# Kernel tuning notes

Measured on AMD Instinct MI355X. Metric: run time of the kernel, lower is better.

The kernel has to match this reference:

```python
import jax, jax.numpy as jnp
import numpy as np

N = 100000   # nodes
E = 1_600_000  # edges (avg degree 16)
D = 64       # input_dim = hidden_dim = output_dim
EPS = 1e-5   # BatchNorm eps


def setup_inputs() -> dict:
    key = jax.random.key(0)
    ks = jax.random.split(key, 8)
    x = jax.random.normal(ks[0], (N, D), jnp.float32)
    edge_index = jax.random.randint(ks[1], (2, E), 0, N, jnp.int32)

    def lin_w(k, din, dout):
        s = 1.0 / np.sqrt(din)
        return jax.random.uniform(k, (din, dout), jnp.float32, -s, s)

    return {
        "x": x, "edge_index": edge_index,
        "W1": lin_w(ks[2], D, D), "b1": jnp.zeros((D,), jnp.float32),
        "g1": jnp.ones((D,), jnp.float32), "be1": jnp.zeros((D,), jnp.float32),
        "W2": lin_w(ks[3], D, D), "b2": jnp.zeros((D,), jnp.float32),
        "g2": jnp.ones((D,), jnp.float32), "be2": jnp.zeros((D,), jnp.float32),
        "W3": lin_w(ks[4], D, D), "b3": jnp.zeros((D,), jnp.float32),
        "g3": jnp.ones((D,), jnp.float32), "be3": jnp.zeros((D,), jnp.float32),
    }


def gcn_conv(x, src, dst, W, b):
    # GCNConv: out = D^{-1/2}(A+I)D^{-1/2} (x @ W) + b
    n = x.shape[0]
    loops = jnp.arange(n, dtype=src.dtype)
    s = jnp.concatenate([src, loops])  # add self-loops
    d = jnp.concatenate([dst, loops])
    deg = jax.ops.segment_sum(jnp.ones_like(s, jnp.float32), d, num_segments=n)
    dinv = jax.lax.rsqrt(jnp.maximum(deg, 1.0))  # deg >= 1 (self-loops)
    norm = dinv[s] * dinv[d]                     # [E+N]
    xw = x @ W                                   # [N, D]
    msgs = xw[s] * norm[:, None]                 # [E+N, D] gather
    return jax.ops.segment_sum(msgs, d, num_segments=n) + b  # scatter-add


def batch_norm(z, g, be):
    # training-mode BatchNorm1d: batch statistics, biased variance
    mu = jnp.mean(z, axis=0)
    var = jnp.mean(jnp.square(z - mu), axis=0)
    return (z - mu) * jax.lax.rsqrt(var + EPS) * g + be


def reference(x, edge_index, W1, b1, g1, be1, W2, b2, g2, be2, W3, b3, g3, be3):
    src, dst = edge_index[0], edge_index[1]
    z = jax.nn.relu(batch_norm(gcn_conv(x, src, dst, W1, b1), g1, be1))
    z = jax.nn.relu(batch_norm(gcn_conv(z, src, dst, W2, b2), g2, be2))
    z = batch_norm(gcn_conv(z, src, dst, W3, b3), g3, be3)
    # dropout (p=0.1) is identity in eval mode; normalize=False default
    return z
```

## Files before the change

### kernel.cpp

```cpp
#include <hip/hip_runtime.h>

typedef unsigned short ushort_t;
typedef unsigned int uint_t;
typedef float f32x4 __attribute__((ext_vector_type(4)));
typedef short bf16x8 __attribute__((ext_vector_type(8)));

#define NB_AGG 2560
#define BSHIFT 7
#define BROWS 128
#define BCAP 4096
#define NCHUNK 256
#define ZP 72

__device__ __forceinline__ float bf2f_lo(uint_t u) {
    union { uint_t i; float f; } v; v.i = u << 16; return v.f;
}
__device__ __forceinline__ float bf2f_hi(uint_t u) {
    union { uint_t i; float f; } v; v.i = u & 0xffff0000u; return v.f;
}
__device__ __forceinline__ ushort_t f2bf(float f) {
    union { float f; uint_t i; } v; v.f = f;
    uint_t u = v.i;
    uint_t r = (u + 0x7fffu + ((u >> 16) & 1u)) >> 16;
    return (ushort_t)r;
}

__global__ __launch_bounds__(256) void hist2_k(const int* __restrict__ dst,
                                               int* __restrict__ H, int E, int nb) {
    __shared__ int h[1024];
    int b = blockIdx.x, t = threadIdx.x;
    for (int i = t; i < nb; i += 256) h[i] = 0;
    __syncthreads();
    int per = (E + NCHUNK - 1) / NCHUNK;
    int lo = b * per, hi = min(E, lo + per);
    for (int e = lo + t; e < hi; e += 256)
        atomicAdd(&h[dst[e] >> BSHIFT], 1);
    __syncthreads();
    for (int i = t; i < nb; i += 256) H[(size_t)i * NCHUNK + b] = h[i];
}

__global__ __launch_bounds__(256) void scanA_k(const int* __restrict__ v,
                                               int* __restrict__ segsum, int total) {
    int base = blockIdx.x * 1024 + threadIdx.x;
    int s = 0;
#pragma unroll
    for (int i = 0; i < 4; ++i) {
        int idx = base + i * 256;
        if (idx < total) s += v[idx];
    }
    __shared__ int sh[256];
    sh[threadIdx.x] = s;
    __syncthreads();
    for (int off = 128; off > 0; off >>= 1) {
        if (threadIdx.x < off) sh[threadIdx.x] += sh[threadIdx.x + off];
        __syncthreads();
    }
    if (threadIdx.x == 0) segsum[blockIdx.x] = sh[0];
}

__global__ void scanB_k(int* segsum, int nseg) {
    __shared__ int sh[256];
    int t = threadIdx.x;
    int own = (t < nseg) ? segsum[t] : 0;
    sh[t] = own;
    __syncthreads();
    for (int off = 1; off < 256; off <<= 1) {
        int v = (t >= off) ? sh[t - off] : 0;
        __syncthreads();
        sh[t] += v;
        __syncthreads();
    }
    if (t < nseg) segsum[t] = sh[t] - own;
}

__global__ __launch_bounds__(256) void scanC2_k(int* __restrict__ H,
                                                const int* __restrict__ segsum,
                                                int total) {
    int t = threadIdx.x;
    int base = blockIdx.x * 1024 + t * 4;
    int c0 = 0, c1 = 0, c2 = 0, c3 = 0;
    if (base + 0 < total) c0 = H[base + 0];
    if (base + 1 < total) c1 = H[base + 1];
    if (base + 2 < total) c2 = H[base + 2];
    if (base + 3 < total) c3 = H[base + 3];
    int tsum = c0 + c1 + c2 + c3;
    __shared__ int sh[256];
    sh[t] = tsum;
    __syncthreads();
    for (int off = 1; off < 256; off <<= 1) {
        int v = (t >= off) ? sh[t - off] : 0;
        __syncthreads();
        sh[t] += v;
        __syncthreads();
    }
    int excl = segsum[blockIdx.x] + sh[t] - tsum;
    if (base + 0 < total) H[base + 0] = excl;
    if (base + 1 < total) H[base + 1] = excl + c0;
    if (base + 2 < total) H[base + 2] = excl + c0 + c1;
    if (base + 3 < total) H[base + 3] = excl + c0 + c1 + c2;
}

__global__ __launch_bounds__(256) void scat2_k(const int* __restrict__ src,
                                               const int* __restrict__ dst,
                                               const int* __restrict__ H,
                                               int* __restrict__ colA, int E, int nb) {
    __shared__ int cur[1024];
    int b = blockIdx.x, t = threadIdx.x;
    for (int i = t; i < nb; i += 256) cur[i] = H[(size_t)i * NCHUNK + b];
    __syncthreads();
    int per = (E + NCHUNK - 1) / NCHUNK;
    int lo = b * per, hi = min(E, lo + per);
    for (int e = lo + t; e < hi; e += 256) {
        int d = dst[e];
        int bk = d >> BSHIFT;
        int pos = atomicAdd(&cur[bk], 1);
        colA[pos] = (src[e] << BSHIFT) | (d & (BROWS - 1));
    }
}

__global__ __launch_bounds__(256) void build_k(int* __restrict__ colA,
                                               const int* __restrict__ H,
                                               float* __restrict__ dinv,
                                               int* __restrict__ rowp,
                                               int N, int E, int nb) {
    __shared__ int recs[BCAP];
    __shared__ int cnt[BROWS], pfx[BROWS], cur[BROWS];
    int b = blockIdx.x, t = threadIdx.x;
    int base = H[(size_t)b * NCHUNK];
    int next = (b + 1 < nb) ? H[(size_t)(b + 1) * NCHUNK] : E;
    int size = next - base;
    if (size > BCAP) size = BCAP;
    int row0 = b << BSHIFT;

    if (t < BROWS) { cnt[t] = 0; cur[t] = 0; }
    __syncthreads();

    for (int i = t; i < size; i += 256) {
        int r = colA[base + i];
        recs[i] = r;
        atomicAdd(&cnt[r & (BROWS - 1)], 1);
    }
    __syncthreads();

    if (t < BROWS) pfx[t] = cnt[t];
    __syncthreads();
    for (int off = 1; off < BROWS; off <<= 1) {
        int u = 0;
        if (t < BROWS && t >= off) u = pfx[t - off];
        __syncthreads();
        if (t < BROWS) pfx[t] += u;
        __syncthreads();
    }
    if (t < BROWS) {
        int row = row0 + t;
        if (row < N) {
            int ex = pfx[t] - cnt[t];
            rowp[row] = base + ex;
            dinv[row] = rsqrtf((float)cnt[t] + 1.0f);
            if (row == N - 1) rowp[N] = base + pfx[t];
        }
    }
    __syncthreads();

    for (int i = t; i < size; i += 256) {
        int r = recs[i];
        int l = r & (BROWS - 1);
        int pos = base + (pfx[l] - cnt[l]) + atomicAdd(&cur[l], 1);
        colA[pos] = r >> BSHIFT;
    }
}

template <int MODE>
__global__ __launch_bounds__(256) void gemm_k(const float* __restrict__ Z,
                                              const float* __restrict__ W,
                                              const float* __restrict__ dinv,
                                              const float* __restrict__ cA,
                                              const float* __restrict__ cC,
                                              ushort_t* __restrict__ XW, int N) {
    __shared__ ushort_t WbT[64 * ZP];
    __shared__ ushort_t Zt[64 * ZP];
    __shared__ ushort_t Ot[4][16 * ZP];
    __shared__ float Al[64], Cl[64], Dl[64];
    int t = threadIdx.x;
    int row0 = blockIdx.x * 64;

    if (t < 64) {
        int r = row0 + t;
        Dl[t] = (r < N) ? dinv[r] : 0.0f;
        if (MODE) { Al[t] = cA[t]; Cl[t] = cC[t]; }
    }
    {
        int col = t & 63, kg = t >> 6;
#pragma unroll
        for (int kk = 0; kk < 16; ++kk) {
            int k = kg * 16 + kk;
            WbT[col * ZP + k] = f2bf(W[k * 64 + col]);
        }
    }
    __syncthreads();

    {
        int r = t >> 2, cg = t & 3;
        int grow = row0 + r;
        const float4* zr = (const float4*)(Z + (size_t)grow * 64 + cg * 16);
#pragma unroll
        for (int q = 0; q < 4; ++q) {
            float4 v;
            if (grow < N) v = zr[q];
            else { v.x = v.y = v.z = v.w = 0.0f; }
            if (MODE) {
                int k = cg * 16 + q * 4;
                v.x = fmaxf(Al[k + 0] * v.x + Cl[k + 0], 0.0f);
                v.y = fmaxf(Al[k + 1] * v.y + Cl[k + 1], 0.0f);
                v.z = fmaxf(Al[k + 2] * v.z + Cl[k + 2], 0.0f);
                v.w = fmaxf(Al[k + 3] * v.w + Cl[k + 3], 0.0f);
            }
            uint2 p;
            p.x = (uint_t)f2bf(v.x) | ((uint_t)f2bf(v.y) << 16);
            p.y = (uint_t)f2bf(v.z) | ((uint_t)f2bf(v.w) << 16);
            *(uint2*)&Zt[r * ZP + cg * 16 + q * 4] = p;
        }
    }
    __syncthreads();

    int wv = t >> 6, lane = t & 63;
    int mrow = lane & 15;
    int kgrp = lane >> 4;

    f32x4 acc0 = {0, 0, 0, 0}, acc1 = {0, 0, 0, 0};
    f32x4 acc2 = {0, 0, 0, 0}, acc3 = {0, 0, 0, 0};
#pragma unroll
    for (int ks = 0; ks < 2; ++ks) {
        bf16x8 a = *(bf16x8*)&Zt[(wv * 16 + mrow) * ZP + ks * 32 + kgrp * 8];
        bf16x8 b0 = *(bf16x8*)&WbT[(0 + mrow) * ZP + ks * 32 + kgrp * 8];
        bf16x8 b1 = *(bf16x8*)&WbT[(16 + mrow) * ZP + ks * 32 + kgrp * 8];
        bf16x8 b2 = *(bf16x8*)&WbT[(32 + mrow) * ZP + ks * 32 + kgrp * 8];
        bf16x8 b3 = *(bf16x8*)&WbT[(48 + mrow) * ZP + ks * 32 + kgrp * 8];
        acc0 = __builtin_amdgcn_mfma_f32_16x16x32_bf16(a, b0, acc0, 0, 0, 0);
        acc1 = __builtin_amdgcn_mfma_f32_16x16x32_bf16(a, b1, acc1, 0, 0, 0);
        acc2 = __builtin_amdgcn_mfma_f32_16x16x32_bf16(a, b2, acc2, 0, 0, 0);
        acc3 = __builtin_amdgcn_mfma_f32_16x16x32_bf16(a, b3, acc3, 0, 0, 0);
    }

#pragma unroll
    for (int r = 0; r < 4; ++r) {
        int orow = kgrp * 4 + r;
        float dn = Dl[wv * 16 + orow];
        Ot[wv][orow * ZP + 0 + mrow]  = f2bf(acc0[r] * dn);
        Ot[wv][orow * ZP + 16 + mrow] = f2bf(acc1[r] * dn);
        Ot[wv][orow * ZP + 32 + mrow] = f2bf(acc2[r] * dn);
        Ot[wv][orow * ZP + 48 + mrow] = f2bf(acc3[r] * dn);
    }
#pragma unroll
    for (int i = 0; i < 2; ++i) {
        int cid = lane * 2 + i;
        int orow = cid >> 3, seg = cid & 7;
        int grow = row0 + wv * 16 + orow;
        if (grow < N)
            *(uint4*)(XW + (size_t)grow * 64 + seg * 8) =
                *(uint4*)&Ot[wv][orow * ZP + seg * 8];
    }
}

__global__ __launch_bounds__(256) void agg_k(const ushort_t* __restrict__ y,
                                             const int* __restrict__ row_ptr,
                                             const int* __restrict__ colA,
                                             const float* __restrict__ dinv,
                                             float* __restrict__ OUT,
                                             float* __restrict__ pS,
                                             float* __restrict__ pQ, int N) {
    __shared__ float ssum[64], ssq[64];
    int t = threadIdx.x, lane = t & 63, wv = t >> 6;
    int g = lane >> 4;
    int c = lane & 15;
    if (t < 64) ssum[t] = 0.0f;
    else if (t < 128) ssq[t - 64] = 0.0f;
    __syncthreads();

    const uint2* y2 = (const uint2*)y;
    float ps0 = 0, ps1 = 0, ps2 = 0, ps3 = 0;
    float pq0 = 0, pq1 = 0, pq2 = 0, pq3 = 0;

    for (int row = blockIdx.x * 4 + wv; row < N; row += NB_AGG * 4) {
        int start = row_ptr[row];
        int end = row_ptr[row + 1];
        float a0 = 0, a1 = 0, a2 = 0, a3 = 0;

        for (int base = start; base < end; base += 32) {
            int sA[8];
            uint_t mA[8];
#pragma unroll
            for (int u = 0; u < 8; ++u) {
                int e = base + u * 4 + g;
                int ec = min(e, end - 1);
                sA[u] = colA[ec];
                mA[u] = (e < end) ? 0xffffffffu : 0u;
            }
#pragma unroll
            for (int u = 0; u < 8; ++u) {
                uint2 v = y2[(size_t)sA[u] * 16 + c];
                v.x &= mA[u]; v.y &= mA[u];
                a0 += bf2f_lo(v.x);
                a1 += bf2f_hi(v.x);
                a2 += bf2f_lo(v.y);
                a3 += bf2f_hi(v.y);
            }
        }

        a0 += __shfl_xor(a0, 16); a0 += __shfl_xor(a0, 32);
        a1 += __shfl_xor(a1, 16); a1 += __shfl_xor(a1, 32);
        a2 += __shfl_xor(a2, 16); a2 += __shfl_xor(a2, 32);
        a3 += __shfl_xor(a3, 16); a3 += __shfl_xor(a3, 32);

        if (g == 0) {
            float dn = dinv[row];
            uint2 sv = y2[(size_t)row * 16 + c];
            float v0 = dn * (a0 + bf2f_lo(sv.x));
            float v1 = dn * (a1 + bf2f_hi(sv.x));
            float v2 = dn * (a2 + bf2f_lo(sv.y));
            float v3 = dn * (a3 + bf2f_hi(sv.y));
            float4 o; o.x = v0; o.y = v1; o.z = v2; o.w = v3;
            *(float4*)(OUT + (size_t)row * 64 + c * 4) = o;
            ps0 += v0; ps1 += v1; ps2 += v2; ps3 += v3;
            pq0 += v0 * v0; pq1 += v1 * v1; pq2 += v2 * v2; pq3 += v3 * v3;
        }
    }

    if (g == 0) {
        atomicAdd(&ssum[c * 4 + 0], ps0); atomicAdd(&ssq[c * 4 + 0], pq0);
        atomicAdd(&ssum[c * 4 + 1], ps1); atomicAdd(&ssq[c * 4 + 1], pq1);
        atomicAdd(&ssum[c * 4 + 2], ps2); atomicAdd(&ssq[c * 4 + 2], pq2);
        atomicAdd(&ssum[c * 4 + 3], ps3); atomicAdd(&ssq[c * 4 + 3], pq3);
    }
    __syncthreads();
    if (t < 64) pS[(size_t)t * NB_AGG + blockIdx.x] = ssum[t];
    else if (t < 128) pQ[(size_t)(t - 64) * NB_AGG + blockIdx.x] = ssq[t - 64];
}

__global__ __launch_bounds__(256) void stats_k(const float* __restrict__ pS,
                                               const float* __restrict__ pQ,
                                               const float* __restrict__ g,
                                               const float* __restrict__ be,
                                               float* __restrict__ cA,
                                               float* __restrict__ cC, int N) {
    int c = blockIdx.x, t = threadIdx.x;
    float s = 0.0f, q = 0.0f;
    for (int i = t; i < NB_AGG; i += 256) {
        s += pS[(size_t)c * NB_AGG + i];
        q += pQ[(size_t)c * NB_AGG + i];
    }
    __shared__ float rs[256], rq[256];
    rs[t] = s; rq[t] = q;
    __syncthreads();
    for (int off = 128; off > 0; off >>= 1) {
        if (t < off) { rs[t] += rs[t + off]; rq[t] += rq[t + off]; }
        __syncthreads();
    }
    if (t == 0) {
        float mu = rs[0] / (float)N;
        float var = rq[0] / (float)N - mu * mu;
        var = fmaxf(var, 0.0f);
        float inv = rsqrtf(var + 1e-5f);
        float a = g[c] * inv;
        cA[c] = a;
        cC[c] = be[c] - mu * a;
    }
}

__global__ __launch_bounds__(256) void apply_k(float* __restrict__ O,
                                               const float* __restrict__ cA,
                                               const float* __restrict__ cC,
                                               int N) {
    int total = N * 16;
    for (int i = blockIdx.x * 256 + threadIdx.x; i < total; i += gridDim.x * 256) {
        float4 v = ((float4*)O)[i];
        int c = (i & 15) * 4;
        v.x = cA[c + 0] * v.x + cC[c + 0];
        v.y = cA[c + 1] * v.y + cC[c + 1];
        v.z = cA[c + 2] * v.z + cC[c + 2];
        v.w = cA[c + 3] * v.w + cC[c + 3];
        ((float4*)O)[i] = v;
    }
}

extern "C" void kernel_launch(void* const* d_in, const int* in_sizes, int n_in,
                              void* d_out, int out_size, void* d_ws, size_t ws_size,
                              hipStream_t stream) {
    const float* x   = (const float*)d_in[0];
    const int*   ei  = (const int*)d_in[1];
    const float* W1  = (const float*)d_in[2];
    const float* g1  = (const float*)d_in[4];
    const float* be1 = (const float*)d_in[5];
    const float* W2  = (const float*)d_in[6];
    const float* g2  = (const float*)d_in[8];
    const float* be2 = (const float*)d_in[9];
    const float* W3  = (const float*)d_in[10];
    const float* g3  = (const float*)d_in[12];
    const float* be3 = (const float*)d_in[13];

    int N = in_sizes[0] / 64;
    int E = in_sizes[1] / 2;
    const int* srcA = ei;
    const int* dstA = ei + E;
    int nb = (N + BROWS - 1) >> BSHIFT;
    int total = nb * NCHUNK;
    int nseg = (total + 1023) / 1024;

    char* w = (char*)d_ws;
    auto alloc = [&](size_t bytes) -> char* {
        char* p = w;
        w += (bytes + 255) & ~(size_t)255;
        return p;
    };
    ushort_t* xw    = (ushort_t*)alloc((size_t)N * 64 * 2);
    int*      rowp  = (int*)alloc(((size_t)N + 1) * 4);
    float*    dinv  = (float*)alloc((size_t)N * 4);
    int*      colA  = (int*)alloc((size_t)E * 4);
    int*      H     = (int*)alloc((size_t)total * 4);
    int*      segsum= (int*)alloc((size_t)nseg * 4);
    float*    pS    = (float*)alloc((size_t)64 * NB_AGG * 4);
    float*    pQ    = (float*)alloc((size_t)64 * NB_AGG * 4);
    float*    cA1 = (float*)alloc(256); float* cC1 = (float*)alloc(256);
    float*    cA2 = (float*)alloc(256); float* cC2 = (float*)alloc(256);
    float*    cA3 = (float*)alloc(256); float* cC3 = (float*)alloc(256);
    (void)ws_size; (void)n_in; (void)out_size;

    float* out = (float*)d_out;

    hist2_k<<<NCHUNK, 256, 0, stream>>>(dstA, H, E, nb);
    scanA_k<<<nseg, 256, 0, stream>>>(H, segsum, total);
    scanB_k<<<1, 256, 0, stream>>>(segsum, nseg);
    scanC2_k<<<nseg, 256, 0, stream>>>(H, segsum, total);
    scat2_k<<<NCHUNK, 256, 0, stream>>>(srcA, dstA, H, colA, E, nb);
    build_k<<<nb, 256, 0, stream>>>(colA, H, dinv, rowp, N, E, nb);

    int gemmGrid = (N + 63) / 64;

    gemm_k<0><<<gemmGrid, 256, 0, stream>>>(x, W1, dinv, nullptr, nullptr, xw, N);
    agg_k<<<NB_AGG, 256, 0, stream>>>(xw, rowp, colA, dinv, out, pS, pQ, N);
    stats_k<<<64, 256, 0, stream>>>(pS, pQ, g1, be1, cA1, cC1, N);

    gemm_k<1><<<gemmGrid, 256, 0, stream>>>(out, W2, dinv, cA1, cC1, xw, N);
    agg_k<<<NB_AGG, 256, 0, stream>>>(xw, rowp, colA, dinv, out, pS, pQ, N);
    stats_k<<<64, 256, 0, stream>>>(pS, pQ, g2, be2, cA2, cC2, N);

    gemm_k<1><<<gemmGrid, 256, 0, stream>>>(out, W3, dinv, cA2, cC2, xw, N);
    agg_k<<<NB_AGG, 256, 0, stream>>>(xw, rowp, colA, dinv, out, pS, pQ, N);
    stats_k<<<64, 256, 0, stream>>>(pS, pQ, g3, be3, cA3, cC3, N);

    apply_k<<<2048, 256, 0, stream>>>(out, cA3, cC3, N);
}
```

Before: 261.0 us.

## Store intermediate layer activations in bf16 and process two rows per wavefront in aggregation

The first two aggregation passes now write their output in bf16 to a separate buffer, and the following GEMM reads that bf16 buffer directly. This halves the bytes for the intermediate activation write and read. The aggregation kernel also splits each 64-lane wavefront into two halves that each handle one row. Each row's neighbours are then gathered 16 at a time instead of 32, which reduces wasted masked lanes at an average degree of 16. The costs are that BN statistics are still taken from the fp32 values while the next layer consumes rounded values, and that the paired rows loop to the longer of the two degrees.

After: 245.3 us. 6.0% less time.

```diff
diff --git a/kernel.cpp b/kernel.cpp
--- a/kernel.cpp
+++ b/kernel.cpp
@@ -171,7 +171,8 @@
 }
 
 template <int MODE>
-__global__ __launch_bounds__(256) void gemm_k(const float* __restrict__ Z,
+__global__ __launch_bounds__(256) void gemm_k(const float* __restrict__ Zf,
+                                              const uint2* __restrict__ Zb,
                                               const float* __restrict__ W,
                                               const float* __restrict__ dinv,
                                               const float* __restrict__ cA,
@@ -202,18 +203,23 @@
     {
         int r = t >> 2, cg = t & 3;
         int grow = row0 + r;
-        const float4* zr = (const float4*)(Z + (size_t)grow * 64 + cg * 16);
+        bool gv = grow < N;
 #pragma unroll
         for (int q = 0; q < 4; ++q) {
             float4 v;
-            if (grow < N) v = zr[q];
-            else { v.x = v.y = v.z = v.w = 0.0f; }
             if (MODE) {
+                uint2 p2 = {0, 0};
+                if (gv) p2 = Zb[(size_t)grow * 16 + cg * 4 + q];
+                v.x = bf2f_lo(p2.x); v.y = bf2f_hi(p2.x);
+                v.z = bf2f_lo(p2.y); v.w = bf2f_hi(p2.y);
                 int k = cg * 16 + q * 4;
                 v.x = fmaxf(Al[k + 0] * v.x + Cl[k + 0], 0.0f);
                 v.y = fmaxf(Al[k + 1] * v.y + Cl[k + 1], 0.0f);
                 v.z = fmaxf(Al[k + 2] * v.z + Cl[k + 2], 0.0f);
                 v.w = fmaxf(Al[k + 3] * v.w + Cl[k + 3], 0.0f);
+            } else {
+                if (gv) v = *(const float4*)(Zf + (size_t)grow * 64 + cg * 16 + q * 4);
+                else { v.x = v.y = v.z = v.w = 0.0f; }
             }
             uint2 p;
             p.x = (uint_t)f2bf(v.x) | ((uint_t)f2bf(v.y) << 16);
@@ -262,16 +268,19 @@
     }
 }
 
+template <int WBF16>
 __global__ __launch_bounds__(256) void agg_k(const ushort_t* __restrict__ y,
                                              const int* __restrict__ row_ptr,
                                              const int* __restrict__ colA,
                                              const float* __restrict__ dinv,
-                                             float* __restrict__ OUT,
+                                             float* __restrict__ OUTF,
+                                             uint2* __restrict__ OUTB,
                                              float* __restrict__ pS,
                                              float* __restrict__ pQ, int N) {
     __shared__ float ssum[64], ssq[64];
     int t = threadIdx.x, lane = t & 63, wv = t >> 6;
-    int g = lane >> 4;
+    int rs = lane >> 5;
+    int g = (lane >> 4) & 1;
     int c = lane & 15;
     if (t < 64) ssum[t] = 0.0f;
     else if (t < 128) ssq[t - 64] = 0.0f;
@@ -281,20 +290,27 @@
     float ps0 = 0, ps1 = 0, ps2 = 0, ps3 = 0;
     float pq0 = 0, pq1 = 0, pq2 = 0, pq3 = 0;
 
-    for (int row = blockIdx.x * 4 + wv; row < N; row += NB_AGG * 4) {
-        int start = row_ptr[row];
-        int end = row_ptr[row + 1];
+    int npair = (N + 1) >> 1;
+    for (int p = blockIdx.x * 4 + wv; p < npair; p += NB_AGG * 4) {
+        int row = p * 2 + rs;
+        bool rv = row < N;
+        int rc = rv ? row : N - 1;
+        int start = row_ptr[rc];
+        int end = row_ptr[rc + 1];
+        int len = rv ? (end - start) : 0;
+        int ml = max(len, __shfl_xor(len, 32));
+
         float a0 = 0, a1 = 0, a2 = 0, a3 = 0;
-
-        for (int base = start; base < end; base += 32) {
+        for (int off = 0; off < ml; off += 16) {
             int sA[8];
             uint_t mA[8];
 #pragma unroll
             for (int u = 0; u < 8; ++u) {
-                int e = base + u * 4 + g;
-                int ec = min(e, end - 1);
+                int slot = off + u * 2 + g;
+                bool val = slot < len;
+                int ec = val ? (start + slot) : 0;
                 sA[u] = colA[ec];
-                mA[u] = (e < end) ? 0xffffffffu : 0u;
+                mA[u] = val ? 0xffffffffu : 0u;
             }
 #pragma unroll
             for (int u = 0; u < 8; ++u) {
@@ -307,20 +323,27 @@
             }
         }
 
-        a0 += __shfl_xor(a0, 16); a0 += __shfl_xor(a0, 32);
-        a1 += __shfl_xor(a1, 16); a1 += __shfl_xor(a1, 32);
-        a2 += __shfl_xor(a2, 16); a2 += __shfl_xor(a2, 32);
-        a3 += __shfl_xor(a3, 16); a3 += __shfl_xor(a3, 32);
-
-        if (g == 0) {
+        a0 += __shfl_xor(a0, 16);
+        a1 += __shfl_xor(a1, 16);
+        a2 += __shfl_xor(a2, 16);
+        a3 += __shfl_xor(a3, 16);
+
+        if (g == 0 && rv) {
             float dn = dinv[row];
             uint2 sv = y2[(size_t)row * 16 + c];
             float v0 = dn * (a0 + bf2f_lo(sv.x));
             float v1 = dn * (a1 + bf2f_hi(sv.x));
             float v2 = dn * (a2 + bf2f_lo(sv.y));
             float v3 = dn * (a3 + bf2f_hi(sv.y));
-            float4 o; o.x = v0; o.y = v1; o.z = v2; o.w = v3;
-            *(float4*)(OUT + (size_t)row * 64 + c * 4) = o;
+            if (WBF16) {
+                uint2 pk;
+                pk.x = (uint_t)f2bf(v0) | ((uint_t)f2bf(v1) << 16);
+                pk.y = (uint_t)f2bf(v2) | ((uint_t)f2bf(v3) << 16);
+                OUTB[(size_t)row * 16 + c] = pk;
+            } else {
+                float4 o; o.x = v0; o.y = v1; o.z = v2; o.w = v3;
+                *(float4*)(OUTF + (size_t)row * 64 + c * 4) = o;
+            }
             ps0 += v0; ps1 += v1; ps2 += v2; ps3 += v3;
             pq0 += v0 * v0; pq1 += v1 * v1; pq2 += v2 * v2; pq3 += v3 * v3;
         }
@@ -413,6 +436,7 @@
         return p;
     };
     ushort_t* xw    = (ushort_t*)alloc((size_t)N * 64 * 2);
+    uint2*    zb    = (uint2*)alloc((size_t)N * 64 * 2);
     int*      rowp  = (int*)alloc(((size_t)N + 1) * 4);
     float*    dinv  = (float*)alloc((size_t)N * 4);
     int*      colA  = (int*)alloc((size_t)E * 4);
@@ -436,16 +460,16 @@
 
     int gemmGrid = (N + 63) / 64;
 
-    gemm_k<0><<<gemmGrid, 256, 0, stream>>>(x, W1, dinv, nullptr, nullptr, xw, N);
-    agg_k<<<NB_AGG, 256, 0, stream>>>(xw, rowp, colA, dinv, out, pS, pQ, N);
+    gemm_k<0><<<gemmGrid, 256, 0, stream>>>(x, nullptr, W1, dinv, nullptr, nullptr, xw, N);
+    agg_k<1><<<NB_AGG, 256, 0, stream>>>(xw, rowp, colA, dinv, nullptr, zb, pS, pQ, N);
     stats_k<<<64, 256, 0, stream>>>(pS, pQ, g1, be1, cA1, cC1, N);
 
-    gemm_k<1><<<gemmGrid, 256, 0, stream>>>(out, W2, dinv, cA1, cC1, xw, N);
-    agg_k<<<NB_AGG, 256, 0, stream>>>(xw, rowp, colA, dinv, out, pS, pQ, N);
+    gemm_k<1><<<gemmGrid, 256, 0, stream>>>(nullptr, zb, W2, dinv, cA1, cC1, xw, N);
+    agg_k<1><<<NB_AGG, 256, 0, stream>>>(xw, rowp, colA, dinv, nullptr, zb, pS, pQ, N);
     stats_k<<<64, 256, 0, stream>>>(pS, pQ, g2, be2, cA2, cC2, N);
 
-    gemm_k<1><<<gemmGrid, 256, 0, stream>>>(out, W3, dinv, cA2, cC2, xw, N);
-    agg_k<<<NB_AGG, 256, 0, stream>>>(xw, rowp, colA, dinv, out, pS, pQ, N);
+    gemm_k<1><<<gemmGrid, 256, 0, stream>>>(nullptr, zb, W3, dinv, cA2, cC2, xw, N);
+    agg_k<0><<<NB_AGG, 256, 0, stream>>>(xw, rowp, colA, dinv, out, nullptr, pS, pQ, N);
     stats_k<<<64, 256, 0, stream>>>(pS, pQ, g3, be3, cA3, cC3, N);
 
     apply_k<<<2048, 256, 0, stream>>>(out, cA3, cC3, N);
```
